# Optimization experiments

Hardware: AMD Instinct MI355X
Metric: run time of the kernel (lower is better)

The kernel has to match this reference:

```python
import jax, jax.numpy as jnp
import numpy as np

H = 16  # num heads


def setup_inputs() -> dict:
    key = jax.random.key(0)
    ks = jax.random.split(key, 12)
    B, S, D = 2, 2048, 1024
    f = lambda k, shape: jax.random.normal(k, shape, dtype=jnp.float32) * 0.02
    return {
        "Q": jax.random.normal(ks[0], (B, S, D), dtype=jnp.float32),
        "K": jax.random.normal(ks[1], (B, S, D), dtype=jnp.float32),
        "V": jax.random.normal(ks[2], (B, S, D), dtype=jnp.float32),
        "mask": jax.random.randint(ks[3], (B, S, S), 0, 2, dtype=jnp.int32),
        "Wq": f(ks[4], (D, D)), "bq": f(ks[5], (D,)),
        "Wk": f(ks[6], (D, D)), "bk": f(ks[7], (D,)),
        "Wv": f(ks[8], (D, D)), "bv": f(ks[9], (D,)),
        "Wo": f(ks[10], (D, D)), "bo": f(ks[11], (D,)),
    }


def mha(Q, K, V, mask, Wq, bq, Wk, bk, Wv, bv, Wo, bo):
    B, S, D = Q.shape
    d_k = D // H
    # torch Linear: x @ W.T + b
    q = (Q @ Wq.T + bq).reshape(B, S, H, d_k).transpose(0, 2, 1, 3)  # [B,H,S,dk]
    k = (K @ Wk.T + bk).reshape(B, S, H, d_k).transpose(0, 2, 1, 3)
    v = (V @ Wv.T + bv).reshape(B, S, H, d_k).transpose(0, 2, 1, 3)
    scores = jnp.einsum('bhqd,bhkd->bhqk', q, k) / jnp.sqrt(jnp.float32(d_k))
    # faithful to torch: mask.repeat(H,1,1) tiles batch-major along dim0 of [B*H,S,S]
    m = jnp.tile(mask, (H, 1, 1)).reshape(B, H, S, S)
    scores = jnp.where(m == 0, jnp.float32(-1e9), scores)
    attn = jax.nn.softmax(scores, axis=-1)                 # [B,H,S,S]
    ctx = jnp.einsum('bhqk,bhkd->bhqd', attn, v)           # [B,H,S,dk]
    ctx = ctx.transpose(0, 2, 1, 3).reshape(B, S, D)
    out = ctx @ Wo.T + bo
    return out, attn


def reference(Q, K, V, mask, Wq, bq, Wk, bk, Wv, bv, Wo, bo):
    return mha(Q, K, V, mask, Wq, bq, Wk, bk, Wv, bv, Wo, bo)
```

## Files before the change

### kernel.cpp

```cpp
#include <hip/hip_runtime.h>
#include <stdint.h>


typedef __attribute__((ext_vector_type(8))) short bf16x8;
typedef __attribute__((ext_vector_type(4))) float f32x4;
typedef unsigned long long u64;

#define MFMA16(a, b, c) __builtin_amdgcn_mfma_f32_16x16x32_bf16((a), (b), (c), 0, 0, 0)

#define GLDS16(g, l)                                                   \
  __builtin_amdgcn_global_load_lds(                                    \
      (const __attribute__((address_space(1))) unsigned int*)(g),      \
      (__attribute__((address_space(3))) unsigned int*)(l), 16, 0, 0)

__device__ __forceinline__ float bf2f(short s) {
  union { float f; unsigned u; } x;
  x.u = ((unsigned)(unsigned short)s) << 16;
  return x.f;
}
__device__ __forceinline__ short f2bf(float f) {
  union { float f; unsigned u; } x;
  x.f = f;
  unsigned r = x.u + 0x7fffu + ((x.u >> 16) & 1u);
  return (short)(r >> 16);
}
__device__ __forceinline__ bf16x8 pack8(float4 a, float4 b) {
  union { short s[8]; bf16x8 v; } u;
  u.s[0] = f2bf(a.x); u.s[1] = f2bf(a.y); u.s[2] = f2bf(a.z); u.s[3] = f2bf(a.w);
  u.s[4] = f2bf(b.x); u.s[5] = f2bf(b.y); u.s[6] = f2bf(b.z); u.s[7] = f2bf(b.w);
  return u.v;
}

__global__ __launch_bounds__(256) void sentinel_fill(float* __restrict__ out,
                                                     float v, int n) {
  int i = blockIdx.x * 256 + threadIdx.x;
  if (i < n) out[i] = v;
}

__global__ __launch_bounds__(256) void pack_mask(const int* __restrict__ m,
                                                 u64* __restrict__ p) {
  long idx = (long)blockIdx.x * 256 + threadIdx.x;
  u64 b = __ballot(m[idx] != 0);
  if ((threadIdx.x & 63) == 0) p[idx >> 6] = b;
}

struct QkvPtrs {
  const float *A0, *A1, *A2;
  const float *W0, *W1, *W2;
  const float *c0, *c1, *c2;
  short *o0, *o1, *o2;
};
__global__ __launch_bounds__(256) void gemm_qkv(QkvPtrs p) {
  __shared__ short As[128 * 32];
  __shared__ short Bs[128 * 32];
  const int z = blockIdx.z;
  const float* Af = z == 0 ? p.A0 : (z == 1 ? p.A1 : p.A2);
  const float* W = z == 0 ? p.W0 : (z == 1 ? p.W1 : p.W2);
  const float* bias = z == 0 ? p.c0 : (z == 1 ? p.c1 : p.c2);
  short* outs = z == 0 ? p.o0 : (z == 1 ? p.o1 : p.o2);

  const int tid = threadIdx.x;
  const int lane = tid & 63;
  const int wid = tid >> 6;
  const int wr = wid >> 1, wc = wid & 1;
  const int m0 = blockIdx.x * 128;
  const int n0 = blockIdx.y * 128;

  const int srow = tid >> 1;
  const int scol = (tid & 1) << 4;
  const long aoff = (long)(m0 + srow) * 1024 + scol;
  const float* Wg = W + (long)(n0 + srow) * 1024 + scol;
  short* sA = As + srow * 32 + scol;
  short* sB = Bs + srow * 32 + scol;

  f32x4 acc[4][4] = {};
  const int fr = lane & 15;
  const int fc = (lane >> 4) << 3;

  for (int k0 = 0; k0 < 1024; k0 += 32) {
    __syncthreads();
    float4 x0 = *(const float4*)(Af + aoff + k0);
    float4 x1 = *(const float4*)(Af + aoff + k0 + 4);
    float4 x2 = *(const float4*)(Af + aoff + k0 + 8);
    float4 x3 = *(const float4*)(Af + aoff + k0 + 12);
    float4 w0 = *(const float4*)(Wg + k0);
    float4 w1 = *(const float4*)(Wg + k0 + 4);
    float4 w2 = *(const float4*)(Wg + k0 + 8);
    float4 w3 = *(const float4*)(Wg + k0 + 12);
    *(bf16x8*)sA = pack8(x0, x1);
    *(bf16x8*)(sA + 8) = pack8(x2, x3);
    *(bf16x8*)sB = pack8(w0, w1);
    *(bf16x8*)(sB + 8) = pack8(w2, w3);
    __syncthreads();
    bf16x8 a[4], b[4];
#pragma unroll
    for (int i = 0; i < 4; ++i)
      a[i] = *(const bf16x8*)&As[(wr * 64 + i * 16 + fr) * 32 + fc];
#pragma unroll
    for (int i = 0; i < 4; ++i)
      b[i] = *(const bf16x8*)&Bs[(wc * 64 + i * 16 + fr) * 32 + fc];
#pragma unroll
    for (int i = 0; i < 4; ++i)
#pragma unroll
      for (int j = 0; j < 4; ++j)
        acc[i][j] = MFMA16(a[i], b[j], acc[i][j]);
  }

#pragma unroll
  for (int i = 0; i < 4; ++i) {
    const int row0 = m0 + wr * 64 + i * 16 + (lane >> 4) * 4;
#pragma unroll
    for (int j = 0; j < 4; ++j) {
      const int col = n0 + wc * 64 + j * 16 + fr;
      const float bv = bias[col];
      const int h = col >> 6, dd = col & 63;
      if (z != 2) {
#pragma unroll
        for (int r = 0; r < 4; ++r) {
          const int m = row0 + r;
          const long o = (((long)(m >> 11) * 16 + h) * 2048 + (m & 2047)) * 64 + dd;
          outs[o] = f2bf(acc[i][j][r] + bv);
        }
      } else {
        const long o = (((long)(row0 >> 11) * 16 + h) * 64 + dd) * 2048 + (row0 & 2047);
        union { unsigned short us[4]; uint2 v; } pk;
#pragma unroll
        for (int r = 0; r < 4; ++r) pk.us[r] = (unsigned short)f2bf(acc[i][j][r] + bv);
        *(uint2*)&outs[o] = pk.v;
      }
    }
  }
}

__global__ __launch_bounds__(256) void gemm_out(const short* __restrict__ Ab,
                                                const float* __restrict__ W,
                                                const float* __restrict__ bias,
                                                float* __restrict__ outf) {
  __shared__ short As[128 * 32];
  __shared__ short Bs[128 * 32];
  const int tid = threadIdx.x;
  const int lane = tid & 63;
  const int wid = tid >> 6;
  const int wr = wid >> 1, wc = wid & 1;
  const int m0 = blockIdx.x * 128;
  const int n0 = blockIdx.y * 128;

  const int srow = tid >> 1;
  const int scol = (tid & 1) << 4;
  const long aoff = (long)(m0 + srow) * 1024 + scol;
  const float* Wg = W + (long)(n0 + srow) * 1024 + scol;
  short* sA = As + srow * 32 + scol;
  short* sB = Bs + srow * 32 + scol;

  f32x4 acc[4][4] = {};
  const int fr = lane & 15;
  const int fc = (lane >> 4) << 3;

  for (int k0 = 0; k0 < 1024; k0 += 32) {
    __syncthreads();
    bf16x8 va0 = *(const bf16x8*)(Ab + aoff + k0);
    bf16x8 va1 = *(const bf16x8*)(Ab + aoff + k0 + 8);
    float4 w0 = *(const float4*)(Wg + k0);
    float4 w1 = *(const float4*)(Wg + k0 + 4);
    float4 w2 = *(const float4*)(Wg + k0 + 8);
    float4 w3 = *(const float4*)(Wg + k0 + 12);
    *(bf16x8*)sA = va0;
    *(bf16x8*)(sA + 8) = va1;
    *(bf16x8*)sB = pack8(w0, w1);
    *(bf16x8*)(sB + 8) = pack8(w2, w3);
    __syncthreads();
    bf16x8 a[4], b[4];
#pragma unroll
    for (int i = 0; i < 4; ++i)
      a[i] = *(const bf16x8*)&As[(wr * 64 + i * 16 + fr) * 32 + fc];
#pragma unroll
    for (int i = 0; i < 4; ++i)
      b[i] = *(const bf16x8*)&Bs[(wc * 64 + i * 16 + fr) * 32 + fc];
#pragma unroll
    for (int i = 0; i < 4; ++i)
#pragma unroll
      for (int j = 0; j < 4; ++j)
        acc[i][j] = MFMA16(a[i], b[j], acc[i][j]);
  }

#pragma unroll
  for (int i = 0; i < 4; ++i) {
    const int row0 = m0 + wr * 64 + i * 16 + (lane >> 4) * 4;
#pragma unroll
    for (int j = 0; j < 4; ++j) {
      const int col = n0 + wc * 64 + j * 16 + fr;
      const float bv = bias[col];
#pragma unroll
      for (int r = 0; r < 4; ++r)
        outf[(long)(row0 + r) * 1024 + col] = acc[i][j][r] + bv;
    }
  }
}

__global__ __launch_bounds__(256) void attn_fused(
    const short* __restrict__ qw, const short* __restrict__ kw,
    const short* __restrict__ vtw, const u64* __restrict__ pm,
    float* __restrict__ attn, short* __restrict__ ctx) {
  __shared__ short Ks[2][4096];
  __shared__ short Vs[2][4096];
  __shared__ short P[4][32 * 72];
  const int tid = threadIdx.x;
  const int lane = tid & 63;
  const int wid = tid >> 6;
  const int bh = blockIdx.x;
  const int mb = bh & 1;
  const int q0 = blockIdx.y * 128 + wid * 32;
  const int fr = lane & 15;
  const int fg = lane >> 4;
  short* Pw = P[wid];

  bf16x8 aq[2][2];
#pragma unroll
  for (int mi = 0; mi < 2; ++mi) {
    const short* qb = qw + ((long)bh * 2048 + q0 + mi * 16 + fr) * 64 + fg * 8;
#pragma unroll
    for (int ks = 0; ks < 2; ++ks) aq[mi][ks] = *(const bf16x8*)(qb + ks * 32);
  }

  const u64* mbase = pm + ((long)mb * 2048 + q0) * 32;
  const short* kbase = kw + (long)bh * 2048 * 64;
  const short* vbase = vtw + (long)bh * 64 * 2048;
  const long arow = (long)bh * 2048 + q0;

  const int sidx0 = tid;
  const int sidx1 = 256 + tid;
  const int sr0 = sidx0 >> 3, ss0 = (sidx0 ^ sr0) & 7;
  const int sr1 = sidx1 >> 3, ss1 = (sidx1 ^ sr1) & 7;
  short* ldst0 = &Ks[0][0] + (long)(wid * 64) * 8;
  short* ldst1 = &Ks[0][0] + (long)(256 + wid * 64) * 8;
  const long kofs = (long)(&Vs[0][0] - &Ks[0][0]);

#define STAGE_K(buf, kt)                                              \
  {                                                                   \
    const short* s_ = kbase + (long)((kt) * 64) * 64;                 \
    GLDS16(s_ + sr0 * 64 + ss0 * 8, ldst0 + (buf) * 4096);            \
    GLDS16(s_ + sr1 * 64 + ss1 * 8, ldst1 + (buf) * 4096);            \
  }
#define STAGE_V(buf, kt)                                              \
  {                                                                   \
    const short* s_ = vbase + (kt) * 64;                              \
    GLDS16(s_ + (long)sr0 * 2048 + ss0 * 8, ldst0 + kofs + (buf) * 4096); \
    GLDS16(s_ + (long)sr1 * 2048 + ss1 * 8, ldst1 + kofs + (buf) * 4096); \
  }
#define SWZ(row, slot) (((row) << 6) + ((((slot) ^ ((row) & 7))) << 3))
#define WRITEBACK(kt)                                                 \
  {                                                                   \
    _Pragma("unroll") for (int c = 0; c < 8; ++c) {                   \
      const int idx = c * 64 + lane;                                  \
      const int row = idx >> 4;                                       \
      const int col = (idx & 15) * 4;                                 \
      union { uint2 w; short s[4]; } v4;                              \
      v4.w = *(const uint2*)&Pw[row * 72 + col];                      \
      float4 f;                                                       \
      f.x = bf2f(v4.s[0]); f.y = bf2f(v4.s[1]);                       \
      f.z = bf2f(v4.s[2]); f.w = bf2f(v4.s[3]);                       \
      *(float4*)&attn[(arow + row) * 2048 + (kt) * 64 + col] = f;     \
    }                                                                 \
  }

  float rs[2] = {0.f, 0.f};
  STAGE_K(0, 0);
  __syncthreads();
  int cur = 0;
  for (int kt = 0; kt < 32; ++kt) {
    if (kt < 31) STAGE_K(cur ^ 1, kt + 1);
    u64 mrow[2];
#pragma unroll
    for (int mi = 0; mi < 2; ++mi)
      mrow[mi] = mbase[(mi * 16 + fr) * 32 + kt];
#pragma unroll
    for (int ni = 0; ni < 4; ++ni) {
      const int R = ni * 16 + fr;
      bf16x8 b0 = *(const bf16x8*)&Ks[cur][SWZ(R, fg)];
      bf16x8 b1 = *(const bf16x8*)&Ks[cur][SWZ(R, 4 + fg)];
      const int kb0 = ni * 16 + fg * 4;
#pragma unroll
      for (int mi = 0; mi < 2; ++mi) {
        f32x4 s = {0.f, 0.f, 0.f, 0.f};
        s = MFMA16(b0, aq[mi][0], s);
        s = MFMA16(b1, aq[mi][1], s);
#pragma unroll
        for (int r = 0; r < 4; ++r)
          if ((mrow[mi] >> (kb0 + r)) & 1ULL) rs[mi] += __expf(s[r] * 0.125f);
      }
    }
    __syncthreads();
    cur ^= 1;
  }
  float il[2];
#pragma unroll
  for (int mi = 0; mi < 2; ++mi) {
    float v = rs[mi];
    v += __shfl_xor(v, 16);
    v += __shfl_xor(v, 32);
    il[mi] = 1.0f / v;
  }

  f32x4 cacc[2][4] = {};
  STAGE_K(0, 0);
  STAGE_V(0, 0);
  __syncthreads();
  cur = 0;
  for (int kt = 0; kt < 32; ++kt) {
    if (kt > 0) WRITEBACK(kt - 1);
    if (kt < 31) {
      STAGE_K(cur ^ 1, kt + 1);
      STAGE_V(cur ^ 1, kt + 1);
    }
    u64 mrow[2];
#pragma unroll
    for (int mi = 0; mi < 2; ++mi)
      mrow[mi] = mbase[(mi * 16 + fr) * 32 + kt];

#pragma unroll
    for (int ni = 0; ni < 4; ++ni) {
      const int R = ni * 16 + fr;
      bf16x8 b0 = *(const bf16x8*)&Ks[cur][SWZ(R, fg)];
      bf16x8 b1 = *(const bf16x8*)&Ks[cur][SWZ(R, 4 + fg)];
      const int kb0 = ni * 16 + fg * 4;
#pragma unroll
      for (int mi = 0; mi < 2; ++mi) {
        f32x4 s = {0.f, 0.f, 0.f, 0.f};
        s = MFMA16(b0, aq[mi][0], s);
        s = MFMA16(b1, aq[mi][1], s);
        union { unsigned short us[4]; uint2 v; } pk;
#pragma unroll
        for (int r = 0; r < 4; ++r) {
          float p = ((mrow[mi] >> (kb0 + r)) & 1ULL)
                        ? __expf(s[r] * 0.125f) * il[mi]
                        : 0.0f;
          pk.us[r] = (unsigned short)f2bf(p);
        }
        *(uint2*)&Pw[(mi * 16 + fr) * 72 + kb0] = pk.v;
      }
    }

#pragma unroll
    for (int ks = 0; ks < 2; ++ks) {
      bf16x8 pa[2];
#pragma unroll
      for (int mi = 0; mi < 2; ++mi)
        pa[mi] = *(const bf16x8*)&Pw[(mi * 16 + fr) * 72 + ks * 32 + fg * 8];
#pragma unroll
      for (int ni = 0; ni < 4; ++ni) {
        const int R = ni * 16 + fr;
        bf16x8 bv = *(const bf16x8*)&Vs[cur][SWZ(R, ks * 4 + fg)];
#pragma unroll
        for (int mi = 0; mi < 2; ++mi)
          cacc[mi][ni] = MFMA16(pa[mi], bv, cacc[mi][ni]);
      }
    }

    __syncthreads();
    cur ^= 1;
  }
  WRITEBACK(31);

  const int b_ = bh >> 4, h_ = bh & 15;
#pragma unroll
  for (int mi = 0; mi < 2; ++mi)
#pragma unroll
    for (int ni = 0; ni < 4; ++ni)
#pragma unroll
      for (int r = 0; r < 4; ++r)
        ctx[((long)b_ * 2048 + q0 + mi * 16 + fg * 4 + r) * 1024 + h_ * 64 +
            ni * 16 + fr] = f2bf(cacc[mi][ni][r]);
#undef STAGE_K
#undef STAGE_V
#undef SWZ
#undef WRITEBACK
}

extern "C" void kernel_launch(void* const* d_in, const int* in_sizes, int n_in,
                              void* d_out, int out_size, void* d_ws,
                              size_t ws_size, hipStream_t stream) {
  float* out_o = (float*)d_out;

  const bool sizes_ok =
      (n_in == 12) && in_sizes[0] == 4194304 && in_sizes[1] == 4194304 &&
      in_sizes[2] == 4194304 && in_sizes[3] == 8388608 &&
      in_sizes[4] == 1048576 && in_sizes[5] == 1024 &&
      in_sizes[10] == 1048576 && in_sizes[11] == 1024 &&
      out_size == (2 * 2048 * 1024 + 2 * 16 * 2048 * 2048);
  const size_t WS_NEED = 34603008;
  if (!sizes_ok) {
    sentinel_fill<<<dim3(16384), 256, 0, stream>>>(out_o, 555.0f, 4194304);
    return;
  }
  if (ws_size < WS_NEED) {
    sentinel_fill<<<dim3(16384), 256, 0, stream>>>(out_o, 777.0f, 4194304);
    return;
  }

  const float* Q = (const float*)d_in[0];
  const float* K = (const float*)d_in[1];
  const float* V = (const float*)d_in[2];
  const int* mask = (const int*)d_in[3];
  const float* Wq = (const float*)d_in[4];
  const float* bq = (const float*)d_in[5];
  const float* Wk = (const float*)d_in[6];
  const float* bk = (const float*)d_in[7];
  const float* Wv = (const float*)d_in[8];
  const float* bv = (const float*)d_in[9];
  const float* Wo = (const float*)d_in[10];
  const float* bo = (const float*)d_in[11];

  short* qws = (short*)d_ws;
  short* kws = qws + 4194304;
  short* vtws = kws + 4194304;
  short* ctxws = vtws + 4194304;
  u64* pmask = (u64*)(ctxws + 4194304);

  float* out_attn = out_o + 2 * 2048 * 1024;

  pack_mask<<<dim3(2 * 2048 * 2048 / 256), 256, 0, stream>>>(mask, pmask);
  QkvPtrs p = {Q, K, V, Wq, Wk, Wv, bq, bk, bv, qws, kws, vtws};
  gemm_qkv<<<dim3(32, 8, 3), 256, 0, stream>>>(p);
  attn_fused<<<dim3(32, 16), 256, 0, stream>>>(qws, kws, vtws, pmask,
                                               out_attn, ctxws);
  gemm_out<<<dim3(32, 8), 256, 0, stream>>>(ctxws, Wo, bo, out_o);
}
```

Before: 382.1 us.

## Halve attention query tile per warp and swizzle P buffer layout

Each warp now handles 16 query rows instead of 32, so each block covers 64 queries and the grid doubles to 1024 blocks. This raises parallelism across the GPU's CUs and lowers register pressure. The P scratch buffer switches from padded rows to an XOR-swizzled 64-column layout to avoid LDS bank conflicts. The cost is that K/V tiles are loaded twice as often overall, because each block reuses them across fewer query rows.

```diff
diff --git a/kernel.cpp b/kernel.cpp
--- a/kernel.cpp
+++ b/kernel.cpp
@@ -203,23 +203,22 @@
     float* __restrict__ attn, short* __restrict__ ctx) {
   __shared__ short Ks[2][4096];
   __shared__ short Vs[2][4096];
-  __shared__ short P[4][32 * 72];
+  __shared__ short P[4][1024];
   const int tid = threadIdx.x;
   const int lane = tid & 63;
   const int wid = tid >> 6;
   const int bh = blockIdx.x;
   const int mb = bh & 1;
-  const int q0 = blockIdx.y * 128 + wid * 32;
+  const int q0 = blockIdx.y * 64 + wid * 16;
   const int fr = lane & 15;
   const int fg = lane >> 4;
   short* Pw = P[wid];
 
-  bf16x8 aq[2][2];
-#pragma unroll
-  for (int mi = 0; mi < 2; ++mi) {
-    const short* qb = qw + ((long)bh * 2048 + q0 + mi * 16 + fr) * 64 + fg * 8;
-#pragma unroll
-    for (int ks = 0; ks < 2; ++ks) aq[mi][ks] = *(const bf16x8*)(qb + ks * 32);
+  bf16x8 aq[2];
+  {
+    const short* qb = qw + ((long)bh * 2048 + q0 + fr) * 64 + fg * 8;
+    aq[0] = *(const bf16x8*)qb;
+    aq[1] = *(const bf16x8*)(qb + 32);
   }
 
   const u64* mbase = pm + ((long)mb * 2048 + q0) * 32;
@@ -248,14 +247,16 @@
     GLDS16(s_ + (long)sr1 * 2048 + ss1 * 8, ldst1 + kofs + (buf) * 4096); \
   }
 #define SWZ(row, slot) (((row) << 6) + ((((slot) ^ ((row) & 7))) << 3))
+#define PADDR(row, col) \
+  (((row) << 6) + (((((col) >> 3) ^ ((row) & 7))) << 3) + ((col) & 7))
 #define WRITEBACK(kt)                                                 \
   {                                                                   \
-    _Pragma("unroll") for (int c = 0; c < 8; ++c) {                   \
+    _Pragma("unroll") for (int c = 0; c < 4; ++c) {                   \
       const int idx = c * 64 + lane;                                  \
       const int row = idx >> 4;                                       \
       const int col = (idx & 15) * 4;                                 \
       union { uint2 w; short s[4]; } v4;                              \
-      v4.w = *(const uint2*)&Pw[row * 72 + col];                      \
+      v4.w = *(const uint2*)&Pw[PADDR(row, col)];                     \
       float4 f;                                                       \
       f.x = bf2f(v4.s[0]); f.y = bf2f(v4.s[1]);                       \
       f.z = bf2f(v4.s[2]); f.w = bf2f(v4.s[3]);                       \
@@ -263,45 +264,38 @@
     }                                                                 \
   }
 
-  float rs[2] = {0.f, 0.f};
+  float rs = 0.f;
   STAGE_K(0, 0);
   __syncthreads();
   int cur = 0;
   for (int kt = 0; kt < 32; ++kt) {
     if (kt < 31) STAGE_K(cur ^ 1, kt + 1);
-    u64 mrow[2];
-#pragma unroll
-    for (int mi = 0; mi < 2; ++mi)
-      mrow[mi] = mbase[(mi * 16 + fr) * 32 + kt];
+    const u64 mrow = mbase[fr * 32 + kt];
 #pragma unroll
     for (int ni = 0; ni < 4; ++ni) {
       const int R = ni * 16 + fr;
       bf16x8 b0 = *(const bf16x8*)&Ks[cur][SWZ(R, fg)];
       bf16x8 b1 = *(const bf16x8*)&Ks[cur][SWZ(R, 4 + fg)];
       const int kb0 = ni * 16 + fg * 4;
-#pragma unroll
-      for (int mi = 0; mi < 2; ++mi) {
-        f32x4 s = {0.f, 0.f, 0.f, 0.f};
-        s = MFMA16(b0, aq[mi][0], s);
-        s = MFMA16(b1, aq[mi][1], s);
-#pragma unroll
-        for (int r = 0; r < 4; ++r)
-          if ((mrow[mi] >> (kb0 + r)) & 1ULL) rs[mi] += __expf(s[r] * 0.125f);
-      }
+      f32x4 s = {0.f, 0.f, 0.f, 0.f};
+      s = MFMA16(b0, aq[0], s);
+      s = MFMA16(b1, aq[1], s);
+#pragma unroll
+      for (int r = 0; r < 4; ++r)
+        if ((mrow >> (kb0 + r)) & 1ULL) rs += __expf(s[r] * 0.125f);
     }
     __syncthreads();
     cur ^= 1;
   }
-  float il[2];
-#pragma unroll
-  for (int mi = 0; mi < 2; ++mi) {
-    float v = rs[mi];
+  float il;
+  {
+    float v = rs;
     v += __shfl_xor(v, 16);
     v += __shfl_xor(v, 32);
-    il[mi] = 1.0f / v;
-  }
-
-  f32x4 cacc[2][4] = {};
+    il = 1.0f / v;
+  }
+
+  f32x4 cacc[4] = {};
   STAGE_K(0, 0);
   STAGE_V(0, 0);
   __syncthreads();
@@ -312,10 +306,7 @@
       STAGE_K(cur ^ 1, kt + 1);
       STAGE_V(cur ^ 1, kt + 1);
     }
-    u64 mrow[2];
-#pragma unroll
-    for (int mi = 0; mi < 2; ++mi)
-      mrow[mi] = mbase[(mi * 16 + fr) * 32 + kt];
+    const u64 mrow = mbase[fr * 32 + kt];
 
 #pragma unroll
     for (int ni = 0; ni < 4; ++ni) {
@@ -323,36 +314,27 @@
       bf16x8 b0 = *(const bf16x8*)&Ks[cur][SWZ(R, fg)];
       bf16x8 b1 = *(const bf16x8*)&Ks[cur][SWZ(R, 4 + fg)];
       const int kb0 = ni * 16 + fg * 4;
-#pragma unroll
-      for (int mi = 0; mi < 2; ++mi) {
-        f32x4 s = {0.f, 0.f, 0.f, 0.f};
-        s = MFMA16(b0, aq[mi][0], s);
-        s = MFMA16(b1, aq[mi][1], s);
-        union { unsigned short us[4]; uint2 v; } pk;
-#pragma unroll
-        for (int r = 0; r < 4; ++r) {
-          float p = ((mrow[mi] >> (kb0 + r)) & 1ULL)
-                        ? __expf(s[r] * 0.125f) * il[mi]
-                        : 0.0f;
-          pk.us[r] = (unsigned short)f2bf(p);
-        }
-        *(uint2*)&Pw[(mi * 16 + fr) * 72 + kb0] = pk.v;
+      f32x4 s = {0.f, 0.f, 0.f, 0.f};
+      s = MFMA16(b0, aq[0], s);
+      s = MFMA16(b1, aq[1], s);
+      union { unsigned short us[4]; uint2 v; } pk;
+#pragma unroll
+      for (int r = 0; r < 4; ++r) {
+        float p = ((mrow >> (kb0 + r)) & 1ULL) ? __expf(s[r] * 0.125f) * il
+                                               : 0.0f;
+        pk.us[r] = (unsigned short)f2bf(p);
       }
+      *(uint2*)&Pw[PADDR(fr, kb0)] = pk.v;
     }
 
 #pragma unroll
     for (int ks = 0; ks < 2; ++ks) {
-      bf16x8 pa[2];
-#pragma unroll
-      for (int mi = 0; mi < 2; ++mi)
-        pa[mi] = *(const bf16x8*)&Pw[(mi * 16 + fr) * 72 + ks * 32 + fg * 8];
+      bf16x8 pa = *(const bf16x8*)&Pw[PADDR(fr, ks * 32 + fg * 8)];
 #pragma unroll
       for (int ni = 0; ni < 4; ++ni) {
         const int R = ni * 16 + fr;
         bf16x8 bv = *(const bf16x8*)&Vs[cur][SWZ(R, ks * 4 + fg)];
-#pragma unroll
-        for (int mi = 0; mi < 2; ++mi)
-          cacc[mi][ni] = MFMA16(pa[mi], bv, cacc[mi][ni]);
+        cacc[ni] = MFMA16(pa, bv, cacc[ni]);
       }
     }
 
@@ -363,16 +345,15 @@
 
   const int b_ = bh >> 4, h_ = bh & 15;
 #pragma unroll
-  for (int mi = 0; mi < 2; ++mi)
-#pragma unroll
-    for (int ni = 0; ni < 4; ++ni)
-#pragma unroll
-      for (int r = 0; r < 4; ++r)
-        ctx[((long)b_ * 2048 + q0 + mi * 16 + fg * 4 + r) * 1024 + h_ * 64 +
-            ni * 16 + fr] = f2bf(cacc[mi][ni][r]);
+  for (int ni = 0; ni < 4; ++ni)
+#pragma unroll
+    for (int r = 0; r < 4; ++r)
+      ctx[((long)b_ * 2048 + q0 + fg * 4 + r) * 1024 + h_ * 64 + ni * 16 + fr] =
+          f2bf(cacc[ni][r]);
 #undef STAGE_K
 #undef STAGE_V
 #undef SWZ
+#undef PADDR
 #undef WRITEBACK
 }
 
@@ -421,7 +402,7 @@
   pack_mask<<<dim3(2 * 2048 * 2048 / 256), 256, 0, stream>>>(mask, pmask);
   QkvPtrs p = {Q, K, V, Wq, Wk, Wv, bq, bk, bv, qws, kws, vtws};
   gemm_qkv<<<dim3(32, 8, 3), 256, 0, stream>>>(p);
-  attn_fused<<<dim3(32, 16), 256, 0, stream>>>(qws, kws, vtws, pmask,
+  attn_fused<<<dim3(32, 32), 256, 0, stream>>>(qws, kws, vtws, pmask,
                                                out_attn, ctxws);
   gemm_out<<<dim3(32, 8), 256, 0, stream>>>(ctxws, Wo, bo, out_o);
 }
```

After: 374.3 us. -2.1%, faster.
